# Optimization experiments

Hardware: AMD Instinct MI355X
Metric: run time of the kernel (lower is better)

## Reference

```python
import jax, jax.numpy as jnp
import numpy as np

B, S, H, R = 2, 4096, 2048, 2048
NB, CW = 16, 4
BW = R // NB


def _block_diag_linear(x, w, b):
    # x: [B,S,R]; w: [NB,BW,BW]; b: [NB,BW]
    xb = x.reshape(x.shape[0], x.shape[1], NB, BW)
    out = jnp.einsum('bsni,nij->bsnj', xb, w) + b
    return out.reshape(x.shape)


def _causal_conv1d(x, conv_w, conv_b):
    # depthwise causal temporal conv: out[t] = sum_i w[i]*x[t-CW+1+i] + b
    xp = jnp.pad(x, ((0, 0), (CW - 1, 0), (0, 0)))
    out = conv_b
    for i in range(CW):
        out = out + conv_w[i] * xp[:, i:i + x.shape[1], :]
    return out


def _rg_lru_scan(x, x_gate_pre, a_gate_pre, a_param):
    gate_x = jax.nn.sigmoid(x_gate_pre)
    gate_a = jax.nn.sigmoid(a_gate_pre)
    log_a = -8.0 * gate_a * jax.nn.softplus(a_param)  # [B,S,R]
    a = jnp.exp(log_a)
    multiplier = jnp.sqrt(-jnp.expm1(2.0 * log_a))  # sqrt(1 - a^2)
    norm_x = x * gate_x * multiplier
    # h_t = a_t * h_{t-1} + norm_x_t via parallel associative scan over time
    def combine(c1, c2):
        a1, b1 = c1
        a2, b2 = c2
        return a1 * a2, a2 * b1 + b2
    _, h = jax.lax.associative_scan(combine, (a, norm_x), axis=1)
    return h


def setup_inputs() -> dict:
    key = jax.random.key(0)
    ks = jax.random.split(key, 9)
    x = jax.random.normal(ks[0], (B, S, H), dtype=jnp.float32)
    W_xy = jax.random.normal(ks[1], (2 * R, H), dtype=jnp.float32) / np.sqrt(H)
    ig_w = jax.random.normal(ks[2], (NB, BW, BW), dtype=jnp.float32) / np.sqrt(BW)
    ig_b = jnp.zeros((NB, BW), dtype=jnp.float32)
    ag_w = jax.random.normal(ks[3], (NB, BW, BW), dtype=jnp.float32) / np.sqrt(BW)
    ag_b = jnp.zeros((NB, BW), dtype=jnp.float32)
    # forget_init: a = a_real in [0.9, 0.999]; a_param = softplus^{-1}(-log(a_real))
    unif = jax.random.uniform(ks[4], (R,), dtype=jnp.float32)
    a_real = 0.5 * jnp.log(unif * (0.999 ** 2 - 0.9 ** 2) + 0.9 ** 2 + 1e-8)
    a_param = jnp.log(jnp.expm1(-a_real))
    conv_w = jax.random.normal(ks[5], (CW, R), dtype=jnp.float32) / np.sqrt(CW * R)
    conv_b = jnp.zeros((R,), dtype=jnp.float32)
    # resid_proj is zero-init in the module; use small random so output is non-trivial
    W_resid = 0.02 * jax.random.normal(ks[6], (H, R), dtype=jnp.float32)
    return {"x": x, "W_xy": W_xy, "ig_w": ig_w, "ig_b": ig_b,
            "ag_w": ag_w, "ag_b": ag_b, "a_param": a_param,
            "conv_w": conv_w, "conv_b": conv_b, "W_resid": W_resid}


def reference(x, W_xy, ig_w, ig_b, ag_w, ag_b, a_param, conv_w, conv_b, W_resid):
    xy = jnp.einsum('bsh,rh->bsr', x, W_xy)  # [B,S,2R]
    xr, y = jnp.split(xy, 2, axis=-1)
    xc = _causal_conv1d(xr, conv_w, conv_b)
    x_gate_pre = _block_diag_linear(xc, ig_w, ig_b)
    a_gate_pre = _block_diag_linear(xc, ag_w, ag_b)
    h = _rg_lru_scan(xc, x_gate_pre, a_gate_pre, a_param)
    out = jnp.einsum('bsr,hr->bsh', jax.nn.gelu(y, approximate=False) * h, W_resid)
    return out
```

## Files before the change

kernel.cpp:

```cpp
#include <hip/hip_runtime.h>
#include <hip/hip_bf16.h>

typedef __hip_bfloat16 bf16;
typedef __attribute__((ext_vector_type(8))) short s16x8;
typedef __attribute__((ext_vector_type(4))) float f32x4;

#define B_ 2
#define S_ 4096
#define H_ 2048
#define R_ 2048
#define M_ 8192
#define NB_ 16
#define BW_ 128
#define CHUNK 64
#define NCH 64

__device__ __forceinline__ short f2b_s(float f) {
    return (short)__builtin_bit_cast(unsigned short, __float2bfloat16(f));
}
__device__ __forceinline__ float b2f_s(short s) {
    unsigned int u = ((unsigned int)(unsigned short)s) << 16;
    return __builtin_bit_cast(float, u);
}
__device__ __forceinline__ float sigm_fast(float x) { return 1.f / (1.f + __expf(-x)); }

__device__ __forceinline__ void async_g2l(const void* g, void* l) {
    __builtin_amdgcn_global_load_lds((const __attribute__((address_space(1))) void*)g,
                                     (__attribute__((address_space(3))) void*)l, 16, 0, 0);
}

__global__ __launch_bounds__(256) void cast_all(const float* __restrict__ x,
                                                const float* __restrict__ wxy,
                                                const float* __restrict__ wres,
                                                bf16* __restrict__ xbf,
                                                bf16* __restrict__ wxyb,
                                                bf16* __restrict__ wresb) {
    int idx = blockIdx.x * 256 + threadIdx.x;
    const float* in; bf16* out; int off;
    if (idx < 2097152)      { in = x;    out = xbf;   off = idx; }
    else if (idx < 3145728) { in = wxy;  out = wxyb;  off = idx - 2097152; }
    else                    { in = wres; out = wresb; off = idx - 3145728; }
    size_t i8 = (size_t)off * 8;
    float4 v0 = *(const float4*)(in + i8);
    float4 v1 = *(const float4*)(in + i8 + 4);
    s16x8 o;
    o[0] = f2b_s(v0.x); o[1] = f2b_s(v0.y); o[2] = f2b_s(v0.z); o[3] = f2b_s(v0.w);
    o[4] = f2b_s(v1.x); o[5] = f2b_s(v1.y); o[6] = f2b_s(v1.z); o[7] = f2b_s(v1.w);
    *(s16x8*)(out + i8) = o;
}

__global__ __launch_bounds__(256) void wcast_T(const float* __restrict__ igw,
                                               const float* __restrict__ agw,
                                               bf16* __restrict__ wT) {
    __shared__ float tile[128 * 129];
    int blk = blockIdx.x;
    int p = blk >> 4, n = blk & 15;
    const float* w = (p ? agw : igw) + (size_t)n * 16384;
    int tid = threadIdx.x;
#pragma unroll
    for (int it = 0; it < 64; ++it) {
        int u = it * 256 + tid;
        tile[(u >> 7) * 129 + (u & 127)] = w[u];
    }
    __syncthreads();
    bf16* o = wT + (size_t)blk * 16384;
#pragma unroll
    for (int it = 0; it < 64; ++it) {
        int u = it * 256 + tid;
        o[u] = __float2bfloat16(tile[(u & 127) * 129 + (u >> 7)]);
    }
}

__global__ __launch_bounds__(256) void sp8_kernel(const float* __restrict__ apar,
                                                  float* __restrict__ sp8) {
    int r = blockIdx.x * 256 + threadIdx.x;
    float ap = apar[r];
    sp8[r] = 8.f * (ap > 20.f ? ap : log1pf(expf(ap)));
}

__device__ __forceinline__ void store_c(float* p, float v) { *p = v; }
__device__ __forceinline__ void store_c(bf16* p, float v) { *p = __float2bfloat16(v); }

template <typename OutT>
__global__ __launch_bounds__(256, 4) void gemm_bt(const bf16* __restrict__ A,
                                                  const bf16* __restrict__ Bm,
                                                  OutT* __restrict__ C,
                                                  int K, int lda, int ldb, int ldc) {
    __shared__ __align__(16) short As[128 * 64];
    __shared__ __align__(16) short Bs[128 * 64];
    const int tid = threadIdx.x;
    const int lane = tid & 63, wave = tid >> 6;
    const int waveM = wave >> 1, waveN = wave & 1;
    const int mBase = blockIdx.y * 128, nBase = blockIdx.x * 128;
    const int fm = lane & 15, q = lane >> 4;

    f32x4 acc[4][4];
#pragma unroll
    for (int i = 0; i < 4; ++i)
#pragma unroll
        for (int j = 0; j < 4; ++j) acc[i][j] = (f32x4){0.f, 0.f, 0.f, 0.f};

    for (int k0 = 0; k0 < K; k0 += 64) {
        __syncthreads();
#pragma unroll
        for (int it = 0; it < 4; ++it) {
            int off = it * 4096 + tid * 16;
            int r = off >> 7;
            int g = ((off & 127) >> 4) ^ (r & 7);
            async_g2l(A + (size_t)(mBase + r) * lda + k0 + g * 8, (char*)As + off);
            async_g2l(Bm + (size_t)(nBase + r) * ldb + k0 + g * 8, (char*)Bs + off);
        }
        __syncthreads();
#pragma unroll
        for (int s = 0; s < 2; ++s) {
            s16x8 af[4], bfr[4];
#pragma unroll
            for (int i = 0; i < 4; ++i) {
                int row = waveM * 64 + i * 16 + fm;
                af[i] = *(const s16x8*)((char*)As + row * 128 + ((((s << 2) + q) ^ (row & 7)) << 4));
                int col = waveN * 64 + i * 16 + fm;
                bfr[i] = *(const s16x8*)((char*)Bs + col * 128 + ((((s << 2) + q) ^ (col & 7)) << 4));
            }
#pragma unroll
            for (int i = 0; i < 4; ++i)
#pragma unroll
                for (int j = 0; j < 4; ++j)
                    acc[i][j] = __builtin_amdgcn_mfma_f32_16x16x32_bf16(af[i], bfr[j], acc[i][j], 0, 0, 0);
        }
    }
#pragma unroll
    for (int i = 0; i < 4; ++i) {
        int rowg = mBase + waveM * 64 + i * 16 + q * 4;
#pragma unroll
        for (int j = 0; j < 4; ++j) {
            int colg = nBase + waveN * 64 + j * 16 + fm;
#pragma unroll
            for (int rr = 0; rr < 4; ++rr)
                store_c(C + (size_t)(rowg + rr) * ldc + colg, acc[i][j][rr]);
        }
    }
}

__global__ __launch_bounds__(256) void gate_kernel(const bf16* __restrict__ xy,
                                                   const float* __restrict__ cw,
                                                   const float* __restrict__ cb,
                                                   const bf16* __restrict__ wT,
                                                   const float* __restrict__ igb,
                                                   const float* __restrict__ agb,
                                                   const float* __restrict__ sp8,
                                                   bf16* __restrict__ la_out,
                                                   bf16* __restrict__ nx_out,
                                                   float* __restrict__ Ach,
                                                   float* __restrict__ Hla) {
    __shared__ __align__(16) short As[64 * 128];
    __shared__ __align__(16) char  Wmem[128 * 256];
    short* Xs   = (short*)Wmem;
    short* Ws   = (short*)Wmem;
    float* a_sh = (float*)Wmem;
    const int n = blockIdx.x;
    const int mBase = blockIdx.y * 64;
    const int tid = threadIdx.x;
    const int lane = tid & 63, wave = tid >> 6;
    const int fm = lane & 15, q = lane >> 4;
    const int t0 = mBase & (S_ - 1);

#pragma unroll
    for (int it = 0; it < 5; ++it) {
        int u = it * 256 + tid;
        if (u < 67 * 16) {
            int rr = u >> 4, gg = u & 15;
            s16x8 v = (s16x8){0, 0, 0, 0, 0, 0, 0, 0};
            if (t0 != 0 || rr >= 3) {
                int m = mBase + rr - 3;
                v = *(const s16x8*)(xy + (size_t)m * 4096 + n * BW_ + gg * 8);
            }
            *(s16x8*)((char*)Xs + u * 16) = v;
        }
    }
    __syncthreads();

    {
        int col = tid & 127, rh = tid >> 7;
        int rbase = n * BW_ + col;
        float w0c = cw[rbase], w1c = cw[R_ + rbase], w2c = cw[2 * R_ + rbase],
              w3c = cw[3 * R_ + rbase];
        float bc = cb[rbase];
        int r0 = rh * 32;
        float xm3 = b2f_s(Xs[(r0 + 0) * 128 + col]);
        float xm2 = b2f_s(Xs[(r0 + 1) * 128 + col]);
        float xm1 = b2f_s(Xs[(r0 + 2) * 128 + col]);
#pragma unroll
        for (int rw = 0; rw < 32; ++rw) {
            int row = r0 + rw;
            float x0 = b2f_s(Xs[(row + 3) * 128 + col]);
            float v = bc + w0c * xm3 + w1c * xm2 + w2c * xm1 + w3c * x0;
            xm3 = xm2; xm2 = xm1; xm1 = x0;
            *(short*)((char*)As + row * 256 + ((((col >> 3)) ^ (row & 15)) << 4) +
                      (col & 7) * 2) = f2b_s(v);
        }
    }
    __syncthreads();

    const bf16* w0 = wT + (size_t)n * 16384;
#pragma unroll
    for (int it = 0; it < 8; ++it) {
        int off = it * 4096 + tid * 16;
        int j = off >> 8;
        int g = ((off & 255) >> 4) ^ (j & 15);
        async_g2l(w0 + j * 128 + g * 8, (char*)Ws + off);
    }
    __syncthreads();

    f32x4 accI[8], accA[8];
#pragma unroll
    for (int jj = 0; jj < 8; ++jj) {
        accI[jj] = (f32x4){0.f, 0.f, 0.f, 0.f};
        accA[jj] = (f32x4){0.f, 0.f, 0.f, 0.f};
    }

    const int row = wave * 16 + fm;
#pragma unroll
    for (int s = 0; s < 4; ++s) {
        s16x8 af = *(const s16x8*)((char*)As + row * 256 + ((((s << 2) + q) ^ (row & 15)) << 4));
#pragma unroll
        for (int jj = 0; jj < 8; ++jj) {
            int wrow = jj * 16 + fm;
            s16x8 bw = *(const s16x8*)((char*)Ws + wrow * 256 + ((((s << 2) + q) ^ (wrow & 15)) << 4));
            accI[jj] = __builtin_amdgcn_mfma_f32_16x16x32_bf16(af, bw, accI[jj], 0, 0, 0);
        }
    }
    __syncthreads();
    const bf16* w1 = wT + (size_t)(NB_ + n) * 16384;
#pragma unroll
    for (int it = 0; it < 8; ++it) {
        int off = it * 4096 + tid * 16;
        int j = off >> 8;
        int g = ((off & 255) >> 4) ^ (j & 15);
        async_g2l(w1 + j * 128 + g * 8, (char*)Ws + off);
    }
    __syncthreads();
#pragma unroll
    for (int s = 0; s < 4; ++s) {
        s16x8 af = *(const s16x8*)((char*)As + row * 256 + ((((s << 2) + q) ^ (row & 15)) << 4));
#pragma unroll
        for (int jj = 0; jj < 8; ++jj) {
            int wrow = jj * 16 + fm;
            s16x8 bw = *(const s16x8*)((char*)Ws + wrow * 256 + ((((s << 2) + q) ^ (wrow & 15)) << 4));
            accA[jj] = __builtin_amdgcn_mfma_f32_16x16x32_bf16(af, bw, accA[jj], 0, 0, 0);
        }
    }
    __syncthreads();

#pragma unroll
    for (int jj = 0; jj < 8; ++jj) {
        int col = jj * 16 + fm;
        int r = n * BW_ + col;
        float bi = igb[r], ba = agb[r];
        float s8 = sp8[r];
#pragma unroll
        for (int rr = 0; rr < 4; ++rr) {
            int rowl = wave * 16 + q * 4 + rr;
            short* slot = (short*)((char*)As + rowl * 256 +
                          ((((col >> 3)) ^ (rowl & 15)) << 4) + (col & 7) * 2);
            float xcv = b2f_s(*slot);
            float xg = accI[jj][rr] + bi;
            float ag = accA[jj][rr] + ba;
            float la = -s8 * sigm_fast(ag);
            float av = __expf(la);
            float t2 = 2.f * la;
            float nem = (t2 > -0.125f)
                ? -t2 * (1.f + t2 * (0.5f + t2 * (0.16666667f + t2 * 0.04166667f)))
                : 1.f - av * av;
            float nxv = xcv * sigm_fast(xg) * sqrtf(nem);
            short nxs = f2b_s(nxv);
            size_t o = (size_t)(mBase + rowl) * R_ + r;
            la_out[o] = __float2bfloat16(la);
            nx_out[o] = __builtin_bit_cast(bf16, (unsigned short)nxs);
            a_sh[rowl * 128 + col] = av;
            *slot = nxs;
        }
    }
    __syncthreads();

    if (tid < 128) {
        int col = tid;
        float h = 0.f, cum = 1.f;
#pragma unroll 4
        for (int t = 0; t < CHUNK; ++t) {
            float a = a_sh[t * 128 + col];
            float nxv = b2f_s(*(const short*)((char*)As + t * 256 +
                              ((((col >> 3)) ^ (t & 15)) << 4) + (col & 7) * 2));
            h = fmaf(a, h, nxv);
            cum *= a;
        }
        int b = mBase >> 12, c = (mBase & (S_ - 1)) >> 6;
        int so = ((b * NCH + c) << 11) + n * BW_ + col;
        Ach[so] = cum;
        Hla[so] = h;
    }
}

__global__ __launch_bounds__(256) void scan_carry(const float* __restrict__ Ach,
                                                  const float* __restrict__ Hla,
                                                  float* __restrict__ carry) {
    int idx = blockIdx.x * 256 + threadIdx.x;
    int r = idx & (R_ - 1), b = idx >> 11;
    float cy = 0.f;
    for (int c = 0; c < NCH; ++c) {
        int o = (b * NCH + c) * R_ + r;
        carry[o] = cy;
        cy = fmaf(Ach[o], cy, Hla[o]);
    }
}

__global__ __launch_bounds__(256) void scan_passB(const bf16* __restrict__ la_buf,
                                                  const bf16* __restrict__ nx_buf,
                                                  const float* __restrict__ carry,
                                                  const bf16* __restrict__ xy,
                                                  bf16* __restrict__ g_out) {
    int bid = blockIdx.x;
    int rt = bid & 7, c = (bid >> 3) & 63, b = bid >> 9;
    int r = rt * 256 + threadIdx.x;
    int m0 = b * S_ + c * CHUNK;
    size_t base = (size_t)m0 * R_ + r;
    const bf16* yp = xy + (size_t)m0 * 4096 + 2048 + r;
    int so = (b * NCH + c) * R_ + r;
    float h = carry[so];
    for (int t = 0; t < CHUNK; ++t) {
        size_t o = base + (size_t)t * R_;
        float a = __expf(__bfloat162float(la_buf[o]));
        float nx = __bfloat162float(nx_buf[o]);
        h = fmaf(a, h, nx);
        float y = __bfloat162float(yp[(size_t)t * 4096]);
        float g = 0.5f * y * (1.f + erff(y * 0.70710678f));
        g_out[o] = __float2bfloat16(g * h);
    }
}

extern "C" void kernel_launch(void* const* d_in, const int* in_sizes, int n_in,
                              void* d_out, int out_size, void* d_ws, size_t ws_size,
                              hipStream_t stream) {
    const float* x    = (const float*)d_in[0];
    const float* Wxy  = (const float*)d_in[1];
    const float* igw  = (const float*)d_in[2];
    const float* igb  = (const float*)d_in[3];
    const float* agw  = (const float*)d_in[4];
    const float* agb  = (const float*)d_in[5];
    const float* apar = (const float*)d_in[6];
    const float* cw   = (const float*)d_in[7];
    const float* cb   = (const float*)d_in[8];
    const float* Wres = (const float*)d_in[9];
    float* out = (float*)d_out;

    char* ws = (char*)d_ws;
    const size_t MiB = (size_t)1 << 20;
    bf16*  xbf   = (bf16*)(ws);
    bf16*  la    = (bf16*)(ws);
    bf16*  wxyb  = (bf16*)(ws + 32 * MiB);
    bf16*  wT    = (bf16*)(ws + 32 * MiB);
    float* sp8   = (float*)(ws + 33 * MiB + 65536);
    bf16*  xy    = (bf16*)(ws + 48 * MiB);
    bf16*  wresb = (bf16*)(ws + 112 * MiB);
    bf16*  g     = (bf16*)(ws + 120 * MiB);
    bf16*  nx    = (bf16*)(ws + 152 * MiB);
    float* Ach   = (float*)(ws + 184 * MiB);
    float* Hla   = (float*)(ws + 185 * MiB);
    float* cyb   = (float*)(ws + 186 * MiB);

    cast_all<<<14336, 256, 0, stream>>>(x, Wxy, Wres, xbf, wxyb, wresb);

    gemm_bt<bf16><<<dim3(32, 64), 256, 0, stream>>>(xbf, wxyb, xy, 2048, 2048, 2048, 4096);

    wcast_T<<<32, 256, 0, stream>>>(igw, agw, wT);
    sp8_kernel<<<8, 256, 0, stream>>>(apar, sp8);

    gate_kernel<<<dim3(NB_, 128), 256, 0, stream>>>(xy, cw, cb, wT, igb, agb, sp8,
                                                    la, nx, Ach, Hla);

    scan_carry<<<16, 256, 0, stream>>>(Ach, Hla, cyb);
    scan_passB<<<1024, 256, 0, stream>>>(la, nx, cyb, xy, g);

    gemm_bt<float><<<dim3(16, 64), 256, 0, stream>>>(g, wresb, out, 2048, 2048, 2048, 2048);
}
```

Measured before the change: 469.6 us.

## Replace 128x128 GEMM with double-buffered 256x256 pipelined MFMA kernel

Replaces the single-buffered 128x128-tile bf16 GEMM with a 256x256-tile, 512-thread kernel that uses 128 KiB of dynamic LDS split into two buffers. Global-to-LDS loads are issued in quarter-tile units interleaved with the MFMA phases, with explicit vmcnt waits, barriers and setprio. The aim is to hide load latency and raise arithmetic intensity per LDS byte for both projection GEMMs. The larger tile halves occupancy and leaves few workgroups for the output GEMM (256 blocks), and the hand-tuned waitcnt counts are fragile.

After: 468.1 us. Within noise of the previous version (-0.3%).

```diff
diff --git a/kernel.cpp b/kernel.cpp
--- a/kernel.cpp
+++ b/kernel.cpp
@@ -82,58 +82,99 @@
 __device__ __forceinline__ void store_c(bf16* p, float v) { *p = __float2bfloat16(v); }
 
 template <typename OutT>
-__global__ __launch_bounds__(256, 4) void gemm_bt(const bf16* __restrict__ A,
+__global__ __launch_bounds__(512, 2) void gemm256(const bf16* __restrict__ A,
                                                   const bf16* __restrict__ Bm,
                                                   OutT* __restrict__ C,
                                                   int K, int lda, int ldb, int ldc) {
-    __shared__ __align__(16) short As[128 * 64];
-    __shared__ __align__(16) short Bs[128 * 64];
+    extern __shared__ __align__(16) char lds[];
     const int tid = threadIdx.x;
     const int lane = tid & 63, wave = tid >> 6;
-    const int waveM = wave >> 1, waveN = wave & 1;
-    const int mBase = blockIdx.y * 128, nBase = blockIdx.x * 128;
+    const int wm = wave >> 2, wn = wave & 3;
     const int fm = lane & 15, q = lane >> 4;
-
-    f32x4 acc[4][4];
-#pragma unroll
-    for (int i = 0; i < 4; ++i)
+    const int mBase = blockIdx.y * 256, nBase = blockIdx.x * 256;
+    const int NT = K >> 6;
+
+    auto stage_unit = [&](int k) {
+        if (k >= 4 * NT) return;
+        const int tt = k >> 2, hh = k & 3;
+        const bf16* src = (hh & 1) ? Bm : A;
+        const int ld = (hh & 1) ? ldb : lda;
+        const int rowBase = (hh & 1) ? nBase : mBase;
+        char* dst = lds + ((tt & 1) << 16) + (hh << 14);
+        const int kcol = tt * 64 + (hh >> 1) * 32;
+#pragma unroll
+        for (int rnd = 0; rnd < 2; ++rnd) {
+            int off = rnd * 8192 + tid * 16;
+            int r = off >> 6;
+            int g = ((off >> 4) & 3) ^ (r & 3);
+            async_g2l(src + (size_t)(rowBase + r) * ld + kcol + g * 8, dst + off);
+        }
+    };
+
+    f32x4 acc[8][4];
+#pragma unroll
+    for (int i = 0; i < 8; ++i)
 #pragma unroll
         for (int j = 0; j < 4; ++j) acc[i][j] = (f32x4){0.f, 0.f, 0.f, 0.f};
 
-    for (int k0 = 0; k0 < K; k0 += 64) {
-        __syncthreads();
-#pragma unroll
-        for (int it = 0; it < 4; ++it) {
-            int off = it * 4096 + tid * 16;
-            int r = off >> 7;
-            int g = ((off & 127) >> 4) ^ (r & 7);
-            async_g2l(A + (size_t)(mBase + r) * lda + k0 + g * 8, (char*)As + off);
-            async_g2l(Bm + (size_t)(nBase + r) * ldb + k0 + g * 8, (char*)Bs + off);
-        }
-        __syncthreads();
-#pragma unroll
-        for (int s = 0; s < 2; ++s) {
-            s16x8 af[4], bfr[4];
-#pragma unroll
-            for (int i = 0; i < 4; ++i) {
-                int row = waveM * 64 + i * 16 + fm;
-                af[i] = *(const s16x8*)((char*)As + row * 128 + ((((s << 2) + q) ^ (row & 7)) << 4));
-                int col = waveN * 64 + i * 16 + fm;
-                bfr[i] = *(const s16x8*)((char*)Bs + col * 128 + ((((s << 2) + q) ^ (col & 7)) << 4));
+#pragma unroll
+    for (int k = 0; k < 6; ++k) stage_unit(k);
+    asm volatile("s_waitcnt vmcnt(8)" ::: "memory");
+    __builtin_amdgcn_s_barrier();
+    __builtin_amdgcn_sched_barrier(0);
+
+    for (int T = 0; T < NT; ++T) {
+        const int buf = T & 1;
+        const char* base = lds + (buf << 16);
+        s16x8 bfr[4];
+#pragma unroll
+        for (int p = 0; p < 4; ++p) {
+            const int ks = p >> 1, sub = p & 1;
+            if (sub == 0) {
+#pragma unroll
+                for (int j = 0; j < 4; ++j) {
+                    int row = wn * 64 + j * 16 + fm;
+                    bfr[j] = *(const s16x8*)(base + 16384 + (ks << 15) + row * 64 +
+                                             ((q ^ (row & 3)) << 4));
+                }
             }
-#pragma unroll
-            for (int i = 0; i < 4; ++i)
+            s16x8 af[4];
+#pragma unroll
+            for (int i2 = 0; i2 < 4; ++i2) {
+                int row = wm * 128 + (sub * 4 + i2) * 16 + fm;
+                af[i2] = *(const s16x8*)(base + (ks << 15) + row * 64 +
+                                         ((q ^ (row & 3)) << 4));
+            }
+            stage_unit(4 * T + 6 + p);
+            __builtin_amdgcn_s_barrier();
+            asm volatile("s_waitcnt lgkmcnt(0)" ::: "memory");
+            __builtin_amdgcn_sched_barrier(0);
+            __builtin_amdgcn_s_setprio(1);
+#pragma unroll
+            for (int i2 = 0; i2 < 4; ++i2)
 #pragma unroll
                 for (int j = 0; j < 4; ++j)
-                    acc[i][j] = __builtin_amdgcn_mfma_f32_16x16x32_bf16(af[i], bfr[j], acc[i][j], 0, 0, 0);
-        }
-    }
-#pragma unroll
-    for (int i = 0; i < 4; ++i) {
-        int rowg = mBase + waveM * 64 + i * 16 + q * 4;
+                    acc[sub * 4 + i2][j] = __builtin_amdgcn_mfma_f32_16x16x32_bf16(
+                        af[i2], bfr[j], acc[sub * 4 + i2][j], 0, 0, 0);
+            __builtin_amdgcn_s_setprio(0);
+            if (p == 1) {
+                if (T < NT - 1) asm volatile("s_waitcnt vmcnt(8)" ::: "memory");
+                else            asm volatile("s_waitcnt vmcnt(0)" ::: "memory");
+            } else if (p == 3) {
+                if (T < NT - 2)       asm volatile("s_waitcnt vmcnt(8)" ::: "memory");
+                else if (T == NT - 2) asm volatile("s_waitcnt vmcnt(4)" ::: "memory");
+            }
+            __builtin_amdgcn_s_barrier();
+            __builtin_amdgcn_sched_barrier(0);
+        }
+    }
+
+#pragma unroll
+    for (int i = 0; i < 8; ++i) {
+        int rowg = mBase + wm * 128 + i * 16 + q * 4;
 #pragma unroll
         for (int j = 0; j < 4; ++j) {
-            int colg = nBase + waveN * 64 + j * 16 + fm;
+            int colg = nBase + wn * 64 + j * 16 + fm;
 #pragma unroll
             for (int rr = 0; rr < 4; ++rr)
                 store_c(C + (size_t)(rowg + rr) * ldc + colg, acc[i][j][rr]);
@@ -369,7 +410,7 @@
 
     cast_all<<<14336, 256, 0, stream>>>(x, Wxy, Wres, xbf, wxyb, wresb);
 
-    gemm_bt<bf16><<<dim3(32, 64), 256, 0, stream>>>(xbf, wxyb, xy, 2048, 2048, 2048, 4096);
+    gemm256<bf16><<<dim3(16, 32), 512, 131072, stream>>>(xbf, wxyb, xy, 2048, 2048, 2048, 4096);
 
     wcast_T<<<32, 256, 0, stream>>>(igw, agw, wT);
     sp8_kernel<<<8, 256, 0, stream>>>(apar, sp8);
@@ -380,5 +421,5 @@
     scan_carry<<<16, 256, 0, stream>>>(Ach, Hla, cyb);
     scan_passB<<<1024, 256, 0, stream>>>(la, nx, cyb, xy, g);
 
-    gemm_bt<float><<<dim3(16, 64), 256, 0, stream>>>(g, wresb, out, 2048, 2048, 2048, 2048);
-}
+    gemm256<float><<<dim3(8, 32), 512, 131072, stream>>>(g, wresb, out, 2048, 2048, 2048, 2048);
+}
```

## Store local chunk scan state so pass B becomes a parallel elementwise fixup

Applied to the files above, without the earlier changes.

The gate kernel now writes each chunk's local recurrence value and cumulative decay product for every timestep during its serial in-chunk scan, replacing the log-decay and normalized-input outputs. Pass B no longer runs a serial 64-step loop per chunk. It becomes a fully parallel, vectorized elementwise kernel computing h = cum*carry + h_local, fused with the GELU gating. This removes the serial dependency and the exp from pass B. In exchange, the gate kernel's stores now come from only 128 threads inside the serial loop, and bf16 rounding of the cumulative product may cost accuracy.

New measurement: 463.5 us. No clear change (-1.3%).

```diff
diff --git a/kernel.cpp b/kernel.cpp
--- a/kernel.cpp
+++ b/kernel.cpp
@@ -148,8 +148,8 @@
                                                    const float* __restrict__ igb,
                                                    const float* __restrict__ agb,
                                                    const float* __restrict__ sp8,
-                                                   bf16* __restrict__ la_out,
-                                                   bf16* __restrict__ nx_out,
+                                                   bf16* __restrict__ hloc_out,
+                                                   bf16* __restrict__ cum_out,
                                                    float* __restrict__ Ach,
                                                    float* __restrict__ Hla) {
     __shared__ __align__(16) short As[64 * 128];
@@ -273,9 +273,6 @@
                 : 1.f - av * av;
             float nxv = xcv * sigm_fast(xg) * sqrtf(nem);
             short nxs = f2b_s(nxv);
-            size_t o = (size_t)(mBase + rowl) * R_ + r;
-            la_out[o] = __float2bfloat16(la);
-            nx_out[o] = __builtin_bit_cast(bf16, (unsigned short)nxs);
             a_sh[rowl * 128 + col] = av;
             *slot = nxs;
         }
@@ -285,6 +282,7 @@
     if (tid < 128) {
         int col = tid;
         float h = 0.f, cum = 1.f;
+        size_t o = (size_t)mBase * R_ + n * BW_ + col;
 #pragma unroll 4
         for (int t = 0; t < CHUNK; ++t) {
             float a = a_sh[t * 128 + col];
@@ -292,6 +290,9 @@
                               ((((col >> 3)) ^ (t & 15)) << 4) + (col & 7) * 2));
             h = fmaf(a, h, nxv);
             cum *= a;
+            hloc_out[o] = __float2bfloat16(h);
+            cum_out[o]  = __float2bfloat16(cum);
+            o += R_;
         }
         int b = mBase >> 12, c = (mBase & (S_ - 1)) >> 6;
         int so = ((b * NCH + c) << 11) + n * BW_ + col;
@@ -306,6 +307,7 @@
     int idx = blockIdx.x * 256 + threadIdx.x;
     int r = idx & (R_ - 1), b = idx >> 11;
     float cy = 0.f;
+#pragma unroll 4
     for (int c = 0; c < NCH; ++c) {
         int o = (b * NCH + c) * R_ + r;
         carry[o] = cy;
@@ -313,28 +315,35 @@
     }
 }
 
-__global__ __launch_bounds__(256) void scan_passB(const bf16* __restrict__ la_buf,
-                                                  const bf16* __restrict__ nx_buf,
+__global__ __launch_bounds__(256) void scan_passB(const bf16* __restrict__ hloc,
+                                                  const bf16* __restrict__ cum,
                                                   const float* __restrict__ carry,
                                                   const bf16* __restrict__ xy,
                                                   bf16* __restrict__ g_out) {
-    int bid = blockIdx.x;
-    int rt = bid & 7, c = (bid >> 3) & 63, b = bid >> 9;
-    int r = rt * 256 + threadIdx.x;
-    int m0 = b * S_ + c * CHUNK;
-    size_t base = (size_t)m0 * R_ + r;
-    const bf16* yp = xy + (size_t)m0 * 4096 + 2048 + r;
-    int so = (b * NCH + c) * R_ + r;
-    float h = carry[so];
-    for (int t = 0; t < CHUNK; ++t) {
-        size_t o = base + (size_t)t * R_;
-        float a = __expf(__bfloat162float(la_buf[o]));
-        float nx = __bfloat162float(nx_buf[o]);
-        h = fmaf(a, h, nx);
-        float y = __bfloat162float(yp[(size_t)t * 4096]);
-        float g = 0.5f * y * (1.f + erff(y * 0.70710678f));
-        g_out[o] = __float2bfloat16(g * h);
-    }
+    int idx = blockIdx.x * 256 + threadIdx.x;
+    int m = idx >> 8;
+    int r = (idx & 255) << 3;
+    int b = m >> 12, c = (m & 4095) >> 6;
+    int so = ((b * NCH + c) << 11) + r;
+    size_t o = (size_t)m * R_ + r;
+    s16x8 hv = *(const s16x8*)(hloc + o);
+    s16x8 cv = *(const s16x8*)(cum + o);
+    float4 cy0 = *(const float4*)(carry + so);
+    float4 cy1 = *(const float4*)(carry + so + 4);
+    s16x8 yv = *(const s16x8*)(xy + (size_t)m * 4096 + 2048 + r);
+    float cya0 = cy0.x, cya1 = cy0.y, cya2 = cy0.z, cya3 = cy0.w;
+    float cya4 = cy1.x, cya5 = cy1.y, cya6 = cy1.z, cya7 = cy1.w;
+    s16x8 g;
+#pragma unroll 8
+    for (int i = 0; i < 8; ++i) {
+        float cy = (i == 0) ? cya0 : (i == 1) ? cya1 : (i == 2) ? cya2 : (i == 3) ? cya3
+                 : (i == 4) ? cya4 : (i == 5) ? cya5 : (i == 6) ? cya6 : cya7;
+        float h = fmaf(b2f_s(cv[i]), cy, b2f_s(hv[i]));
+        float y = b2f_s(yv[i]);
+        float gg = 0.5f * y * (1.f + erff(y * 0.70710678f));
+        g[i] = f2b_s(gg * h);
+    }
+    *(s16x8*)(g_out + o) = g;
 }
 
 extern "C" void kernel_launch(void* const* d_in, const int* in_sizes, int n_in,
@@ -355,14 +364,14 @@
     char* ws = (char*)d_ws;
     const size_t MiB = (size_t)1 << 20;
     bf16*  xbf   = (bf16*)(ws);
-    bf16*  la    = (bf16*)(ws);
+    bf16*  hloc  = (bf16*)(ws);
     bf16*  wxyb  = (bf16*)(ws + 32 * MiB);
     bf16*  wT    = (bf16*)(ws + 32 * MiB);
     float* sp8   = (float*)(ws + 33 * MiB + 65536);
     bf16*  xy    = (bf16*)(ws + 48 * MiB);
     bf16*  wresb = (bf16*)(ws + 112 * MiB);
     bf16*  g     = (bf16*)(ws + 120 * MiB);
-    bf16*  nx    = (bf16*)(ws + 152 * MiB);
+    bf16*  cum   = (bf16*)(ws + 152 * MiB);
     float* Ach   = (float*)(ws + 184 * MiB);
     float* Hla   = (float*)(ws + 185 * MiB);
     float* cyb   = (float*)(ws + 186 * MiB);
@@ -375,10 +384,10 @@
     sp8_kernel<<<8, 256, 0, stream>>>(apar, sp8);
 
     gate_kernel<<<dim3(NB_, 128), 256, 0, stream>>>(xy, cw, cb, wT, igb, agb, sp8,
-                                                    la, nx, Ach, Hla);
+                                                    hloc, cum, Ach, Hla);
 
     scan_carry<<<16, 256, 0, stream>>>(Ach, Hla, cyb);
-    scan_passB<<<1024, 256, 0, stream>>>(la, nx, cyb, xy, g);
+    scan_passB<<<8192, 256, 0, stream>>>(hloc, cum, cyb, xy, g);
 
     gemm_bt<float><<<dim3(16, 64), 256, 0, stream>>>(g, wresb, out, 2048, 2048, 2048, 2048);
 }
```
